# Performance work log

Hardware: AMD Instinct MI355X
Metric: run time of the kernel (lower is better)

The kernel has to match this reference:

```python
import jax, jax.numpy as jnp
import numpy as np

B, IN, OUT = 512, 4096, 11008


def setup_inputs() -> dict:
    key = jax.random.key(0)
    k_x, k_stored, k_sign, k_scale, k_bias = jax.random.split(key, 5)
    x = jax.random.normal(k_x, (B, IN), dtype=jnp.float32)
    # QINS encoding: stored uint8 magnitude in [1, 255], sign in {-1, +1}
    stored = jax.random.randint(k_stored, (OUT, IN), 1, 256, dtype=jnp.int32)
    sign = 2 * jax.random.randint(k_sign, (OUT, IN), 0, 2, dtype=jnp.int32) - 1
    # log-range from from_linear's fallback calibration: weights in [e^-10, e^0]
    log_min = jnp.asarray(-10.0, dtype=jnp.float32)
    log_max = jnp.asarray(0.0, dtype=jnp.float32)
    # per-channel calibration scale, clamped to [0.5, 2.0] in from_linear
    scale = jax.random.uniform(k_scale, (OUT,), dtype=jnp.float32, minval=0.5, maxval=2.0)
    bias = jax.random.normal(k_bias, (OUT,), dtype=jnp.float32) * 0.01
    return {"x": x, "stored": stored, "sign": sign, "log_min": log_min,
            "log_max": log_max, "scale": scale, "bias": bias}


def reference(x, stored, sign, log_min, log_max, scale, bias):
    # Reconstruct fp32 weight from log-scale uint8 encoding (QINS)
    normalized = (255.0 - stored.astype(jnp.float32)) / 254.0      # [OUT, IN]
    log_w = log_min + normalized * (log_max - log_min)
    weight = sign.astype(jnp.float32) * jnp.exp(log_w)             # [OUT, IN]
    # y = (x @ W^T + b) * scale   (per-output-channel scale)
    out = jnp.einsum('bi,oi->bo', x, weight) + bias
    return out * scale
```

## Files before the change

kernel.cpp:

```cpp
#include <hip/hip_runtime.h>
#include <hip/hip_bf16.h>

#define B_DIM   512
#define IN_DIM  4096
#define OUT_DIM 11008

typedef __bf16 bf16x4 __attribute__((ext_vector_type(4)));
typedef __bf16 bf16x8 __attribute__((ext_vector_type(8)));
typedef float  floatx4 __attribute__((ext_vector_type(4)));

__global__ __launch_bounds__(256) void decode_w_kernel(
    const int* __restrict__ stored, const int* __restrict__ sign,
    const float* __restrict__ logmin, const float* __restrict__ logmax,
    __bf16* __restrict__ w) {
  int idx = blockIdx.x * blockDim.x + threadIdx.x;
  float lmin  = logmin[0];
  float slope = (logmax[0] - lmin) * (1.0f / 254.0f);
  int4 s = ((const int4*)stored)[idx];
  int4 g = ((const int4*)sign)[idx];
  float w0 = __expf(lmin + (float)(255 - s.x) * slope) * (float)g.x;
  float w1 = __expf(lmin + (float)(255 - s.y) * slope) * (float)g.y;
  float w2 = __expf(lmin + (float)(255 - s.z) * slope) * (float)g.z;
  float w3 = __expf(lmin + (float)(255 - s.w) * slope) * (float)g.w;
  bf16x4 o;
  o[0] = (__bf16)w0; o[1] = (__bf16)w1; o[2] = (__bf16)w2; o[3] = (__bf16)w3;
  ((bf16x4*)w)[idx] = o;
}

__global__ __launch_bounds__(256) void conv_x_kernel(
    const float* __restrict__ x, __bf16* __restrict__ xb) {
  int idx = blockIdx.x * blockDim.x + threadIdx.x;
  float4 v = ((const float4*)x)[idx];
  bf16x4 o;
  o[0] = (__bf16)v.x; o[1] = (__bf16)v.y; o[2] = (__bf16)v.z; o[3] = (__bf16)v.w;
  ((bf16x4*)xb)[idx] = o;
}

__device__ __forceinline__ void gl_lds16(const __bf16* g, __bf16* l) {
  __builtin_amdgcn_global_load_lds(
      (const __attribute__((address_space(1))) void*)g,
      (__attribute__((address_space(3))) void*)l, 16, 0, 0);
}

__global__ __launch_bounds__(256, 2) void gemm_bt_kernel(
    const __bf16* __restrict__ A,
    const __bf16* __restrict__ Bw,
    const float* __restrict__ scale, const float* __restrict__ bias,
    float* __restrict__ out) {
  constexpr int K = IN_DIM, N = OUT_DIM;
  constexpr int BM = 128, BN = 128, BK = 32;

  __shared__ __align__(16) __bf16 sA[BM * BK];
  __shared__ __align__(16) __bf16 sB[BN * BK];

  const int tid  = threadIdx.x;
  const int lane = tid & 63;
  const int wave = tid >> 6;
  const int wm   = (wave >> 1) * 64;
  const int wn   = (wave & 1) * 64;
  const int m16  = lane & 15;
  const int q    = lane >> 4;

  const int bn0 = blockIdx.x * BN;
  const int bm0 = blockIdx.y * BM;

  const int r0 = tid >> 2;
  const int c0 = (tid & 3) * 8;
  const __bf16* gA0 = A  + (bm0 + r0) * K + c0;
  const __bf16* gA1 = A  + (bm0 + r0 + 64) * K + c0;
  const __bf16* gB0 = Bw + (bn0 + r0) * K + c0;
  const __bf16* gB1 = Bw + (bn0 + r0 + 64) * K + c0;
  __bf16* lA0 = sA + tid * 8;
  __bf16* lA1 = sA + 2048 + tid * 8;
  __bf16* lB0 = sB + tid * 8;
  __bf16* lB1 = sB + 2048 + tid * 8;

  floatx4 acc[4][4] = {};

  for (int kt = 0; kt < K; kt += BK) {
    __syncthreads();
    gl_lds16(gA0 + kt, lA0);
    gl_lds16(gA1 + kt, lA1);
    gl_lds16(gB0 + kt, lB0);
    gl_lds16(gB1 + kt, lB1);
    __syncthreads();

    bf16x8 afr[4], bfr[4];
#pragma unroll
    for (int i = 0; i < 4; ++i)
      afr[i] = *(const bf16x8*)&sA[(wm + i * 16 + m16) * BK + q * 8];
#pragma unroll
    for (int i = 0; i < 4; ++i)
      bfr[i] = *(const bf16x8*)&sB[(wn + i * 16 + m16) * BK + q * 8];

#pragma unroll
    for (int mi = 0; mi < 4; ++mi)
#pragma unroll
      for (int ni = 0; ni < 4; ++ni)
        acc[mi][ni] = __builtin_amdgcn_mfma_f32_16x16x32_bf16(
            afr[mi], bfr[ni], acc[mi][ni], 0, 0, 0);
  }

#pragma unroll
  for (int ni = 0; ni < 4; ++ni) {
    const int col = bn0 + wn + ni * 16 + m16;
    const float sc = scale[col];
    const float bb = bias[col] * sc;
#pragma unroll
    for (int mi = 0; mi < 4; ++mi) {
#pragma unroll
      for (int r = 0; r < 4; ++r) {
        const int row = bm0 + wm + mi * 16 + q * 4 + r;
        out[row * N + col] = acc[mi][ni][r] * sc + bb;
      }
    }
  }
}

extern "C" void kernel_launch(void* const* d_in, const int* in_sizes, int n_in,
                              void* d_out, int out_size, void* d_ws, size_t ws_size,
                              hipStream_t stream) {
  const float* x      = (const float*)d_in[0];
  const int*   stored = (const int*)d_in[1];
  const int*   sign   = (const int*)d_in[2];
  const float* logmin = (const float*)d_in[3];
  const float* logmax = (const float*)d_in[4];
  const float* scale  = (const float*)d_in[5];
  const float* bias   = (const float*)d_in[6];
  float* out = (float*)d_out;

  __bf16* wsW = (__bf16*)d_ws;
  __bf16* wsX = wsW + (size_t)OUT_DIM * IN_DIM;

  decode_w_kernel<<<(OUT_DIM * (IN_DIM / 4)) / 256, 256, 0, stream>>>(
      stored, sign, logmin, logmax, wsW);
  conv_x_kernel<<<(B_DIM * (IN_DIM / 4)) / 256, 256, 0, stream>>>(x, wsX);
  gemm_bt_kernel<<<dim3(OUT_DIM / 128, B_DIM / 128), 256, 0, stream>>>(
      wsX, wsW, scale, bias, out);
}
```

Measured before the change: 467.8 us.

## Fuse QINS weight decode into GEMM B-tile loading with XCD-aware tile swizzle

Removes the separate weight-decode kernel and its bf16 weight buffer. The GEMM now loads int32 stored/sign values into registers, decodes them with exp, and writes the bf16 tile to LDS each K-step. The A tile is double-buffered in LDS and the next step's loads are prefetched before compute. Workgroups are remapped so the four M-tiles that share a weight column block run on the same XCD and can reuse it in L2. In exchange, each weight element's exp is recomputed in four workgroups and more int data is streamed through the GEMM loop.

```diff
diff --git a/kernel.cpp b/kernel.cpp
--- a/kernel.cpp
+++ b/kernel.cpp
@@ -8,24 +8,6 @@
 typedef __bf16 bf16x4 __attribute__((ext_vector_type(4)));
 typedef __bf16 bf16x8 __attribute__((ext_vector_type(8)));
 typedef float  floatx4 __attribute__((ext_vector_type(4)));
-
-__global__ __launch_bounds__(256) void decode_w_kernel(
-    const int* __restrict__ stored, const int* __restrict__ sign,
-    const float* __restrict__ logmin, const float* __restrict__ logmax,
-    __bf16* __restrict__ w) {
-  int idx = blockIdx.x * blockDim.x + threadIdx.x;
-  float lmin  = logmin[0];
-  float slope = (logmax[0] - lmin) * (1.0f / 254.0f);
-  int4 s = ((const int4*)stored)[idx];
-  int4 g = ((const int4*)sign)[idx];
-  float w0 = __expf(lmin + (float)(255 - s.x) * slope) * (float)g.x;
-  float w1 = __expf(lmin + (float)(255 - s.y) * slope) * (float)g.y;
-  float w2 = __expf(lmin + (float)(255 - s.z) * slope) * (float)g.z;
-  float w3 = __expf(lmin + (float)(255 - s.w) * slope) * (float)g.w;
-  bf16x4 o;
-  o[0] = (__bf16)w0; o[1] = (__bf16)w1; o[2] = (__bf16)w2; o[3] = (__bf16)w3;
-  ((bf16x4*)w)[idx] = o;
-}
 
 __global__ __launch_bounds__(256) void conv_x_kernel(
     const float* __restrict__ x, __bf16* __restrict__ xb) {
@@ -42,16 +24,28 @@
       (__attribute__((address_space(3))) void*)l, 16, 0, 0);
 }
 
-__global__ __launch_bounds__(256, 2) void gemm_bt_kernel(
+__device__ __forceinline__ void memfence_barrier() {
+  asm volatile("" ::: "memory");
+  __builtin_amdgcn_s_barrier();
+  asm volatile("" ::: "memory");
+}
+
+__device__ __forceinline__ __bf16 dec1(int s, int g, float lmin, float slope) {
+  return (__bf16)(__expf(lmin + (float)(255 - s) * slope) * (float)g);
+}
+
+__global__ __launch_bounds__(256, 2) void fused_qins_gemm_kernel(
     const __bf16* __restrict__ A,
-    const __bf16* __restrict__ Bw,
+    const int* __restrict__ stored,
+    const int* __restrict__ sign,
+    const float* __restrict__ logmin, const float* __restrict__ logmax,
     const float* __restrict__ scale, const float* __restrict__ bias,
     float* __restrict__ out) {
   constexpr int K = IN_DIM, N = OUT_DIM;
-  constexpr int BM = 128, BN = 128, BK = 32;
+  constexpr int BK = 32;
 
-  __shared__ __align__(16) __bf16 sA[BM * BK];
-  __shared__ __align__(16) __bf16 sB[BN * BK];
+  __shared__ __align__(16) __bf16 sA[2 * 128 * BK];
+  __shared__ __align__(16) __bf16 sB[128 * BK];
 
   const int tid  = threadIdx.x;
   const int lane = tid & 63;
@@ -61,34 +55,79 @@
   const int m16  = lane & 15;
   const int q    = lane >> 4;
 
-  const int bn0 = blockIdx.x * BN;
-  const int bm0 = blockIdx.y * BM;
+  const int wg  = blockIdx.x;
+  const int g   = (wg & 7) * 43 + (wg >> 3);
+  const int bn0 = (g >> 2) * 128;
+  const int bm0 = (g & 3) * 128;
+
+  const float lmin  = logmin[0];
+  const float slope = (logmax[0] - lmin) * (1.0f / 254.0f);
 
   const int r0 = tid >> 2;
   const int c0 = (tid & 3) * 8;
-  const __bf16* gA0 = A  + (bm0 + r0) * K + c0;
-  const __bf16* gA1 = A  + (bm0 + r0 + 64) * K + c0;
-  const __bf16* gB0 = Bw + (bn0 + r0) * K + c0;
-  const __bf16* gB1 = Bw + (bn0 + r0 + 64) * K + c0;
-  __bf16* lA0 = sA + tid * 8;
-  __bf16* lA1 = sA + 2048 + tid * 8;
-  __bf16* lB0 = sB + tid * 8;
-  __bf16* lB1 = sB + 2048 + tid * 8;
+  const __bf16* gA0 = A + (bm0 + r0) * K + c0;
+  const __bf16* gA1 = A + (bm0 + r0 + 64) * K + c0;
+
+  const int rB = tid >> 1;
+  const int kh = (tid & 1) * 16;
+  const int* pS = stored + (size_t)(bn0 + rB) * K + kh;
+  const int* pG = sign   + (size_t)(bn0 + rB) * K + kh;
+  __bf16* lB = sB + rB * BK + kh;
 
   floatx4 acc[4][4] = {};
 
+  gl_lds16(gA0, sA + tid * 8);
+  gl_lds16(gA1, sA + 2048 + tid * 8);
+  int4 s0 = ((const int4*)pS)[0], s1 = ((const int4*)pS)[1],
+       s2 = ((const int4*)pS)[2], s3 = ((const int4*)pS)[3];
+  int4 g0 = ((const int4*)pG)[0], g1 = ((const int4*)pG)[1],
+       g2 = ((const int4*)pG)[2], g3 = ((const int4*)pG)[3];
+
   for (int kt = 0; kt < K; kt += BK) {
-    __syncthreads();
-    gl_lds16(gA0 + kt, lA0);
-    gl_lds16(gA1 + kt, lA1);
-    gl_lds16(gB0 + kt, lB0);
-    gl_lds16(gB1 + kt, lB1);
-    __syncthreads();
+    const int cur = (kt >> 5) & 1;
+    __bf16* sAc = sA + cur * 4096;
+    __bf16* sAn = sA + (cur ^ 1) * 4096;
+
+    bf16x8 w0, w1;
+    w0[0] = dec1(s0.x, g0.x, lmin, slope);
+    w0[1] = dec1(s0.y, g0.y, lmin, slope);
+    w0[2] = dec1(s0.z, g0.z, lmin, slope);
+    w0[3] = dec1(s0.w, g0.w, lmin, slope);
+    w0[4] = dec1(s1.x, g1.x, lmin, slope);
+    w0[5] = dec1(s1.y, g1.y, lmin, slope);
+    w0[6] = dec1(s1.z, g1.z, lmin, slope);
+    w0[7] = dec1(s1.w, g1.w, lmin, slope);
+    w1[0] = dec1(s2.x, g2.x, lmin, slope);
+    w1[1] = dec1(s2.y, g2.y, lmin, slope);
+    w1[2] = dec1(s2.z, g2.z, lmin, slope);
+    w1[3] = dec1(s2.w, g2.w, lmin, slope);
+    w1[4] = dec1(s3.x, g3.x, lmin, slope);
+    w1[5] = dec1(s3.y, g3.y, lmin, slope);
+    w1[6] = dec1(s3.z, g3.z, lmin, slope);
+    w1[7] = dec1(s3.w, g3.w, lmin, slope);
+
+    memfence_barrier();
+
+    *(bf16x8*)lB       = w0;
+    *(bf16x8*)(lB + 8) = w1;
+
+    asm volatile("s_waitcnt vmcnt(0) lgkmcnt(0)" ::: "memory");
+
+    if (kt + BK < K) {
+      gl_lds16(gA0 + kt + BK, sAn + tid * 8);
+      gl_lds16(gA1 + kt + BK, sAn + 2048 + tid * 8);
+      const int4* nS = (const int4*)(pS + kt + BK);
+      const int4* nG = (const int4*)(pG + kt + BK);
+      s0 = nS[0]; s1 = nS[1]; s2 = nS[2]; s3 = nS[3];
+      g0 = nG[0]; g1 = nG[1]; g2 = nG[2]; g3 = nG[3];
+    }
+
+    memfence_barrier();
 
     bf16x8 afr[4], bfr[4];
 #pragma unroll
     for (int i = 0; i < 4; ++i)
-      afr[i] = *(const bf16x8*)&sA[(wm + i * 16 + m16) * BK + q * 8];
+      afr[i] = *(const bf16x8*)&sAc[(wm + i * 16 + m16) * BK + q * 8];
 #pragma unroll
     for (int i = 0; i < 4; ++i)
       bfr[i] = *(const bf16x8*)&sB[(wn + i * 16 + m16) * BK + q * 8];
@@ -129,12 +168,9 @@
   const float* bias   = (const float*)d_in[6];
   float* out = (float*)d_out;
 
-  __bf16* wsW = (__bf16*)d_ws;
-  __bf16* wsX = wsW + (size_t)OUT_DIM * IN_DIM;
+  __bf16* wsX = (__bf16*)d_ws;
 
-  decode_w_kernel<<<(OUT_DIM * (IN_DIM / 4)) / 256, 256, 0, stream>>>(
-      stored, sign, logmin, logmax, wsW);
-  conv_x_kernel<<<(B_DIM * (IN_DIM / 4)) / 256, 256, 0, stream>>>(x, wsX);
-  gemm_bt_kernel<<<dim3(OUT_DIM / 128, B_DIM / 128), 256, 0, stream>>>(
-      wsX, wsW, scale, bias, out);
+  conv_x_kernel<<<2048, 256, 0, stream>>>(x, wsX);
+  fused_qins_gemm_kernel<<<344, 256, 0, stream>>>(
+      wsX, stored, sign, logmin, logmax, scale, bias, out);
 }
```

Result: slower. 516.8 us (+10.5%).
